# Kernel tuning notes

Hardware: AMD Instinct MI355X
Metric: run time of the kernel (lower is better)

Reference implementation:

```python
import jax, jax.numpy as jnp
import numpy as np
from jax import lax

B, N, C = 16, 16384, 90      # batch, anchors, classes
K = 100                      # per-class pre-NMS top-k
MAX_DET = 100                # final detections per image
IOU_THR = 0.5
SCORE_THR = 0.05


def setup_inputs() -> dict:
    key = jax.random.key(0)
    k1, k2, k3, k4 = jax.random.split(key, 4)
    box_encodings = jax.random.normal(k1, (B, N, 4), dtype=jnp.float32) * 0.5
    class_logits = jax.random.normal(k2, (B, N, C), dtype=jnp.float32) * 2.0 - 3.0
    # anchors as [ymin,xmin,ymax,xmax] in normalized coords
    centers = jax.random.uniform(k3, (N, 2), dtype=jnp.float32)             # (cy,cx)
    sizes = jax.random.uniform(k4, (N, 2), dtype=jnp.float32, minval=0.05, maxval=0.3)
    anchors = jnp.concatenate([centers - sizes / 2, centers + sizes / 2], axis=-1)
    return {"box_encodings": box_encodings, "class_logits": class_logits, "anchors": anchors}


def decode_boxes(enc, anchors):
    ymin, xmin, ymax, xmax = [anchors[:, i] for i in range(4)]
    ha, wa = ymax - ymin, xmax - xmin
    cya, cxa = (ymin + ymax) / 2, (xmin + xmax) / 2
    ty, tx, th, tw = enc[..., 0] / 10.0, enc[..., 1] / 10.0, enc[..., 2] / 5.0, enc[..., 3] / 5.0
    cy = ty * ha + cya
    cx = tx * wa + cxa
    h = jnp.exp(th) * ha
    w = jnp.exp(tw) * wa
    boxes = jnp.stack([cy - h / 2, cx - w / 2, cy + h / 2, cx + w / 2], axis=-1)
    return jnp.clip(boxes, 0.0, 1.0)  # [..., N, 4]


def pairwise_iou(b):  # b: [K,4]
    area = jnp.maximum(b[:, 2] - b[:, 0], 0) * jnp.maximum(b[:, 3] - b[:, 1], 0)
    iy = jnp.maximum(jnp.minimum(b[:, None, 2], b[None, :, 2]) - jnp.maximum(b[:, None, 0], b[None, :, 0]), 0)
    ix = jnp.maximum(jnp.minimum(b[:, None, 3], b[None, :, 3]) - jnp.maximum(b[:, None, 1], b[None, :, 1]), 0)
    inter = iy * ix
    union = area[:, None] + area[None, :] - inter
    return inter / jnp.maximum(union, 1e-8)


def nms_one_class(boxes, scores_c):  # boxes [N,4], scores_c [N]
    vals, idx = lax.top_k(scores_c, K)           # sorted descending
    bk = boxes[idx]                               # [K,4]
    iou = pairwise_iou(bk)                        # [K,K]
    def step(keep, i):
        supp = jnp.any(keep & (iou[i] >= IOU_THR))
        ki = (vals[i] > SCORE_THR) & (~supp)
        return keep.at[i].set(ki), None
    keep, _ = lax.scan(step, jnp.zeros((K,), bool), jnp.arange(K))
    return bk, vals * keep                        # suppressed -> score 0


def postprocess_one(boxes, scores):  # boxes [N,4], scores [N,C]
    bx_ck, sc_ck = jax.vmap(nms_one_class, in_axes=(None, 1))(boxes, scores)  # [C,K,4],[C,K]
    cls_ck = jnp.broadcast_to(jnp.arange(C, dtype=jnp.float32)[:, None], (C, K))
    sc_f = sc_ck.reshape(-1)
    fsc, fidx = lax.top_k(sc_f, MAX_DET)
    fbx = bx_ck.reshape(-1, 4)[fidx]
    fcl = cls_ck.reshape(-1)[fidx]
    return jnp.concatenate([fbx, fcl[:, None], fsc[:, None]], axis=-1)  # [MAX_DET, 6]


def reference(box_encodings, class_logits, anchors):
    boxes = decode_boxes(box_encodings, anchors)       # [B,N,4]
    scores = jax.nn.sigmoid(class_logits)              # [B,N,C]
    combined = jax.vmap(postprocess_one)(boxes, scores)  # [B,MAX_DET,6] = boxes|class|score
    return combined
```

## Files before the change

kernel.cpp:

```cpp
#include <hip/hip_runtime.h>
#include <stdint.h>
#include <math.h>

#define B_ 16
#define NN 16384
#define C_ 90
#define KSEL 100
#define MAXD 100
#define MFLAT (C_ * KSEL)
#define NPAIR 128
#define ZKEY 0x80000000u


__device__ __forceinline__ uint32_t fkey(float f) {
  uint32_t u = __float_as_uint(f);
  return (u & 0x80000000u) ? ~u : (u | 0x80000000u);
}
__device__ __forceinline__ float keyinv(uint32_t k) {
  uint32_t u = (k & 0x80000000u) ? (k & 0x7FFFFFFFu) : ~k;
  return __uint_as_float(u);
}

__device__ __forceinline__ uint32_t blockSum512(uint32_t v, uint32_t* red, uint32_t* s_total) {
  int tid = threadIdx.x;
#pragma unroll
  for (int o = 32; o > 0; o >>= 1) v += __shfl_down(v, o, 64);
  if ((tid & 63) == 0) red[tid >> 6] = v;
  __syncthreads();
  if (tid == 0) {
    uint32_t s = 0;
#pragma unroll
    for (int i = 0; i < 8; ++i) s += red[i];
    *s_total = s;
  }
  __syncthreads();
  return *s_total;
}

__device__ __forceinline__ uint32_t blockSum256(uint32_t v, uint32_t* red, uint32_t* s_total) {
  int tid = threadIdx.x;
#pragma unroll
  for (int o = 32; o > 0; o >>= 1) v += __shfl_down(v, o, 64);
  if ((tid & 63) == 0) red[tid >> 6] = v;
  __syncthreads();
  if (tid == 0) *s_total = red[0] + red[1] + red[2] + red[3];
  __syncthreads();
  return *s_total;
}

__global__ __launch_bounds__(256) void transpose_key16_kernel(const float* __restrict__ logits,
                                                              uint16_t* __restrict__ keys16T) {
  __shared__ uint32_t tile[128 * 91];
  int b = blockIdx.y;
  int n0 = blockIdx.x * 128;
  const float4* src4 = reinterpret_cast<const float4*>(logits + ((size_t)b * NN + n0) * C_);
  for (int p = threadIdx.x; p < 2880; p += 256) {
    float4 v = src4[p];
    int e = p * 4;
    float vv[4] = {v.x, v.y, v.z, v.w};
#pragma unroll
    for (int j = 0; j < 4; ++j) {
      int ee = e + j;
      tile[(ee / C_) * 91 + (ee % C_)] = fkey(vv[j]);
    }
  }
  __syncthreads();
  uint16_t* dstb = keys16T + (size_t)b * C_ * NN + n0;
  for (int q = threadIdx.x; q < C_ * 16; q += 256) {
    int c = q >> 4, g = q & 15;
    int nn2 = g * 8;
    uint4 o;
    o.x = (tile[(nn2 + 0) * 91 + c] >> 16) | (tile[(nn2 + 1) * 91 + c] & 0xFFFF0000u);
    o.y = (tile[(nn2 + 2) * 91 + c] >> 16) | (tile[(nn2 + 3) * 91 + c] & 0xFFFF0000u);
    o.z = (tile[(nn2 + 4) * 91 + c] >> 16) | (tile[(nn2 + 5) * 91 + c] & 0xFFFF0000u);
    o.w = (tile[(nn2 + 6) * 91 + c] >> 16) | (tile[(nn2 + 7) * 91 + c] & 0xFFFF0000u);
    reinterpret_cast<uint4*>(dstb + (size_t)c * NN)[g] = o;
  }
}

template <int TR>
__global__ __launch_bounds__(512, 4) void select_kernel(
    const uint16_t* __restrict__ keys16T,
    const float* __restrict__ logits,
    uint32_t* __restrict__ candPacked,
    uint32_t* __restrict__ candCount) {
  __shared__ uint32_t hist[2048];
  __shared__ uint32_t sc[512];
  __shared__ uint32_t ws8[64];
  __shared__ int s_bsel;
  __shared__ uint32_t s_Sincl, s_Sexcl;
  __shared__ uint32_t red[8];
  __shared__ uint32_t s_total;
  __shared__ uint32_t s_cnt;

  const int c = blockIdx.x, b = blockIdx.y;
  const int tid = threadIdx.x;

  uint32_t keyw[16];
  if (TR) {
    const uint4* src4 = reinterpret_cast<const uint4*>(keys16T + ((size_t)b * C_ + c) * NN);
#pragma unroll
    for (int q = 0; q < 4; ++q) {
      uint4 kv = src4[q * 512 + tid];
      keyw[4 * q + 0] = kv.x; keyw[4 * q + 1] = kv.y;
      keyw[4 * q + 2] = kv.z; keyw[4 * q + 3] = kv.w;
    }
  } else {
    const float* src = logits + (size_t)b * NN * C_ + c;
#pragma unroll
    for (int m = 0; m < 16; ++m) {
      uint32_t i0 = (uint32_t)((((m >> 2) * 512 + tid) * 8) + ((m & 3) * 2));
      uint32_t klo = fkey(src[(size_t)i0 * C_]) >> 16;
      uint32_t khi = fkey(src[(size_t)(i0 + 1) * C_]) >> 16;
      keyw[m] = klo | (khi << 16);
    }
  }

  reinterpret_cast<uint4*>(hist)[tid] = make_uint4(0u, 0u, 0u, 0u);
  __syncthreads();
#pragma unroll
  for (int m = 0; m < 16; ++m) {
    uint32_t w = keyw[m];
    atomicAdd(&hist[(w & 0xFFFFu) >> 5], 1u);
    atomicAdd(&hist[w >> 21], 1u);
  }
  __syncthreads();

  uint32_t m_above = 0;
  uint32_t need = 100u;
  uint32_t cut16 = 0;
  int found = 0;
  int tiepath = 0;
  uint32_t V16 = 0, Texact = NN - 1;

  {
    uint32_t h0 = hist[4 * tid], h1 = hist[4 * tid + 1];
    uint32_t h2 = hist[4 * tid + 2], h3 = hist[4 * tid + 3];
    sc[tid] = h0 + h1 + h2 + h3;
    if (tid == 0) s_bsel = -1;
    __syncthreads();
    if (tid < 64) {
      uint32_t w = 0;
      int base = tid * 8;
#pragma unroll
      for (int i = 0; i < 8; ++i) w += sc[base + i];
#pragma unroll
      for (int off = 1; off < 64; off <<= 1) {
        uint32_t v = __shfl_down(w, off, 64);
        if (tid + off < 64) w += v;
      }
      ws8[tid] = w;
    }
    __syncthreads();
    {
      int g = tid >> 3;
      uint32_t above = (g < 63) ? ws8[g + 1] : 0u;
      for (int j = (g << 3) + 7; j > tid; --j) above += sc[j];
      uint32_t run = above;
      int best = -1;
      uint32_t bi = 0, be = 0;
      uint32_t hh[4] = {h0, h1, h2, h3};
#pragma unroll
      for (int p = 3; p >= 0; --p) {
        uint32_t h = hh[p];
        run += h;
        if (best < 0 && run >= need) { best = 4 * tid + p; bi = run; be = run - h; }
      }
      if (best >= 0) atomicMax(&s_bsel, best);
      __syncthreads();
      if (best >= 0 && best == s_bsel) { s_Sincl = bi; s_Sexcl = be; }
    }
    __syncthreads();

    uint32_t bsel = (uint32_t)s_bsel;
    uint32_t Sincl = s_Sincl, Sexcl = s_Sexcl;
    if (Sincl <= (uint32_t)NPAIR) {
      cut16 = bsel << 5;
      found = 1;
    } else {
      m_above = Sexcl;
      need = 100u - m_above;
      __syncthreads();
      if (tid < 8) reinterpret_cast<uint4*>(hist)[tid] = make_uint4(0u, 0u, 0u, 0u);
      __syncthreads();
#pragma unroll
      for (int m = 0; m < 16; ++m) {
        uint32_t w = keyw[m];
        uint32_t klo = w & 0xFFFFu, khi = w >> 16;
        if ((klo >> 5) == bsel) atomicAdd(&hist[klo & 31u], 1u);
        if ((khi >> 5) == bsel) atomicAdd(&hist[khi & 31u], 1u);
      }
      __syncthreads();
      uint32_t run = 0;
      int b1 = -1;
      uint32_t Si = 0, Se = 0;
      for (int p = 31; p >= 0; --p) {
        uint32_t h = hist[p];
        run += h;
        if (b1 < 0 && run >= need) { b1 = p; Si = run; Se = run - h; }
      }
      uint32_t cutv = (bsel << 5) | (uint32_t)b1;
      if (m_above + Si <= (uint32_t)NPAIR) {
        cut16 = cutv;
        found = 1;
      } else {
        tiepath = 1;
        V16 = cutv;
        m_above += Se;
        uint32_t r = 100u - m_above;
        uint32_t lo2 = 0, hi2 = NN - 1;
        while (lo2 < hi2) {
          uint32_t mid2 = lo2 + ((hi2 - lo2) >> 1);
          uint32_t cnt = 0;
#pragma unroll
          for (int m = 0; m < 16; ++m) {
            uint32_t w = keyw[m];
            uint32_t i0 = (uint32_t)((((m >> 2) * 512 + tid) * 8) + ((m & 3) * 2));
            cnt += ((w & 0xFFFFu) == V16 && i0 <= mid2) ? 1u : 0u;
            cnt += ((w >> 16) == V16 && (i0 + 1) <= mid2) ? 1u : 0u;
          }
          uint32_t tot = blockSum512(cnt, red, &s_total);
          if (tot >= r) hi2 = mid2; else lo2 = mid2 + 1;
        }
        Texact = lo2;
      }
    }
  }

  if (tid == 0) s_cnt = 0;
  __syncthreads();
  uint32_t* outp = candPacked + (size_t)(b * C_ + c) * NPAIR;
#pragma unroll
  for (int m = 0; m < 16; ++m) {
    uint32_t w = keyw[m];
    uint32_t i0 = (uint32_t)((((m >> 2) * 512 + tid) * 8) + ((m & 3) * 2));
    uint32_t klo = w & 0xFFFFu, khi = w >> 16;
    bool t0 = tiepath ? (klo > V16 || (klo == V16 && i0 <= Texact)) : (klo >= cut16);
    bool t1 = tiepath ? (khi > V16 || (khi == V16 && (i0 + 1) <= Texact)) : (khi >= cut16);
    if (t0) {
      uint32_t p = atomicAdd(&s_cnt, 1u);
      if (p < (uint32_t)NPAIR) outp[p] = (klo << 16) | i0;
    }
    if (t1) {
      uint32_t p = atomicAdd(&s_cnt, 1u);
      if (p < (uint32_t)NPAIR) outp[p] = (khi << 16) | (i0 + 1);
    }
  }
  __syncthreads();
  if (tid == 0) candCount[b * C_ + c] = (s_cnt > (uint32_t)NPAIR) ? (uint32_t)NPAIR : s_cnt;
}

__global__ __launch_bounds__(128, 4) void sort_nms_kernel(
    const uint32_t* __restrict__ candPacked,
    const uint32_t* __restrict__ candCount,
    const float* __restrict__ logits,
    const float* __restrict__ enc,
    const float* __restrict__ anchors,
    float* __restrict__ candBox,
    float* __restrict__ candScore) {
  __shared__ unsigned long long ck[NPAIR];
  __shared__ float s_vals[KSEL];
  __shared__ float s_boxv[KSEL][5];
  __shared__ float s_area[KSEL];
  __shared__ uint32_t smask[KSEL][4];
  __shared__ unsigned long long s_keepw[2];

  const int c = blockIdx.x, b = blockIdx.y;
  const int tid = threadIdx.x;
  const int bc = b * C_ + c;

  uint32_t cnt = candCount[bc];
  unsigned long long ckv = 0ull;
  if (tid < (int)cnt) {
    uint32_t v = candPacked[(size_t)bc * NPAIR + tid];
    int n = (int)(v & 0x3FFFu);
    float x = logits[((size_t)b * NN + n) * C_ + c];
    float s = 1.0f / (1.0f + expf(-x));
    ckv = ((unsigned long long)fkey(s) << 32) | (unsigned long long)(~(uint32_t)n);
  }
  ck[tid] = ckv;
  __syncthreads();

  for (int kk = 2; kk <= 128; kk <<= 1) {
    for (int j = kk >> 1; j > 0; j >>= 1) {
      int ixj = tid ^ j;
      if (ixj > tid) {
        unsigned long long a = ck[tid], bb2 = ck[ixj];
        if ((a < bb2) == ((tid & kk) == 0)) { ck[tid] = bb2; ck[ixj] = a; }
      }
      __syncthreads();
    }
  }

  if (tid < KSEL) {
    unsigned long long keyv = ck[tid];
    uint32_t hk = (uint32_t)(keyv >> 32);
    int n = (int)(~(uint32_t)(keyv & 0xFFFFFFFFull)) & (NN - 1);
    s_vals[tid] = keyinv(hk);
    float4 e = reinterpret_cast<const float4*>(enc)[(size_t)b * NN + n];
    float4 a = reinterpret_cast<const float4*>(anchors)[n];
    float ha = a.z - a.x, wa = a.w - a.y;
    float cya = (a.x + a.z) * 0.5f, cxa = (a.y + a.w) * 0.5f;
    float cy = (e.x / 10.0f) * ha + cya;
    float cx = (e.y / 10.0f) * wa + cxa;
    float h = expf(e.z / 5.0f) * ha;
    float w = expf(e.w / 5.0f) * wa;
    float y1 = fminf(fmaxf(cy - h * 0.5f, 0.0f), 1.0f);
    float x1 = fminf(fmaxf(cx - w * 0.5f, 0.0f), 1.0f);
    float y2 = fminf(fmaxf(cy + h * 0.5f, 0.0f), 1.0f);
    float x2 = fminf(fmaxf(cx + w * 0.5f, 0.0f), 1.0f);
    s_boxv[tid][0] = y1; s_boxv[tid][1] = x1; s_boxv[tid][2] = y2; s_boxv[tid][3] = x2;
    s_area[tid] = fmaxf(y2 - y1, 0.0f) * fmaxf(x2 - x1, 0.0f);
    smask[tid][0] = 0; smask[tid][1] = 0; smask[tid][2] = 0; smask[tid][3] = 0;
  }
  __syncthreads();

  for (int p = tid; p < (KSEL * (KSEL - 1)) / 2; p += 128) {
    int j = (int)((1.0f + sqrtf(1.0f + 8.0f * (float)p)) * 0.5f);
    while (j * (j - 1) / 2 > p) --j;
    while ((j + 1) * j / 2 <= p) ++j;
    int i = p - j * (j - 1) / 2;
    float iy1 = s_boxv[i][0], ix1 = s_boxv[i][1], iy2 = s_boxv[i][2], ix2 = s_boxv[i][3];
    float jy1 = s_boxv[j][0], jx1 = s_boxv[j][1], jy2 = s_boxv[j][2], jx2 = s_boxv[j][3];
    float ta = fmaxf(fminf(iy2, jy2) - fmaxf(iy1, jy1), 0.0f) *
               fmaxf(fminf(ix2, jx2) - fmaxf(ix1, jx1), 0.0f);
    float un = fmaxf(s_area[i] + s_area[j] - ta, 1e-8f);
    if (ta / un >= 0.5f) atomicOr(&smask[i][j >> 5], 1u << (j & 31));
  }
  __syncthreads();

  if (tid < 64) {
    int L = tid;
    unsigned long long r0 = (unsigned long long)smask[L][0] |
                            ((unsigned long long)smask[L][1] << 32);
    unsigned long long r1 = (unsigned long long)smask[L][2] |
                            ((unsigned long long)smask[L][3] << 32);
    unsigned long long r2 = 0, r3 = 0;
    if (L < KSEL - 64) {
      r2 = (unsigned long long)smask[L + 64][0] | ((unsigned long long)smask[L + 64][1] << 32);
      r3 = (unsigned long long)smask[L + 64][2] | ((unsigned long long)smask[L + 64][3] << 32);
    }
    unsigned long long vm0 = __ballot(s_vals[L] > 0.05f);
    unsigned long long vm1 = __ballot((L + 64 < KSEL) ? (s_vals[L + 64] > 0.05f) : false);
    unsigned long long supp0 = 0, supp1 = 0, k0 = 0, k1 = 0;
    for (int j = 0; j < KSEL; ++j) {
      unsigned long long rl, rh;
      bool pass;
      if (j < 64) {
        rl = __shfl(r0, j); rh = __shfl(r1, j);
        pass = ((vm0 >> j) & 1ull) && !((supp0 >> j) & 1ull);
      } else {
        rl = __shfl(r2, j - 64); rh = __shfl(r3, j - 64);
        pass = ((vm1 >> (j - 64)) & 1ull) && !((supp1 >> (j - 64)) & 1ull);
      }
      if (pass) {
        supp0 |= rl; supp1 |= rh;
        if (j < 64) k0 |= 1ull << j; else k1 |= 1ull << (j - 64);
      }
    }
    if (tid == 0) { s_keepw[0] = k0; s_keepw[1] = k1; }
  }
  __syncthreads();

  if (tid < KSEL) {
    bool kept = (tid < 64) ? ((s_keepw[0] >> tid) & 1ull)
                           : ((s_keepw[1] >> (tid - 64)) & 1ull);
    size_t base = (size_t)bc * KSEL + tid;
    candScore[base] = kept ? s_vals[tid] : 0.0f;
    float* cb = candBox + base * 4;
    cb[0] = s_boxv[tid][0]; cb[1] = s_boxv[tid][1];
    cb[2] = s_boxv[tid][2]; cb[3] = s_boxv[tid][3];
  }
}

#define FSLOT 36
__global__ __launch_bounds__(256) void final_topk_kernel(
    const float* __restrict__ candScore,
    const float* __restrict__ candBox,
    float* __restrict__ out) {
  __shared__ uint32_t hist[2048 * 8];
  __shared__ uint32_t sc[256];
  __shared__ uint32_t ws4[64];
  __shared__ int s_bsel;
  __shared__ uint32_t s_Sincl, s_Sexcl;
  __shared__ uint32_t red[4];
  __shared__ uint32_t s_total;
  __shared__ uint32_t s_cnt;
  __shared__ unsigned long long ck[128];

  int b = blockIdx.x, tid = threadIdx.x;
  const float* src = candScore + (size_t)b * MFLAT;

  uint32_t key[FSLOT];
#pragma unroll
  for (int q = 0; q < FSLOT; ++q) {
    int idx = q * 256 + tid;
    key[q] = (idx < MFLAT) ? fkey(src[idx]) : 0u;
  }

  uint32_t nzc = 0;
#pragma unroll
  for (int q = 0; q < FSLOT; ++q) nzc += (key[q] > ZKEY) ? 1u : 0u;
  uint32_t nz = blockSum256(nzc, red, &s_total);

  uint32_t cutHi = 0, m_above = 0, cut32 = 0;
  int found = 0, tiepath = 0;
  uint32_t V32 = 0, Texact = (uint32_t)(MFLAT - 1);
  uint32_t tie_r = 0;

  if (nz < 100u) {
    tiepath = 1;
    V32 = ZKEY;
    tie_r = 100u - nz;
  } else {
    const int stripe = tid & 7;
    for (int lvl = 0; lvl < 3; ++lvl) {
      const int shiftLo = (lvl == 0) ? 21 : (lvl == 1) ? 10 : 0;
      const uint32_t mask = (lvl == 2) ? 0x3FFu : 0x7FFu;
      const int nbits = (lvl == 2) ? 10 : 11;

      for (int i = tid; i < 4096; i += 256)
        reinterpret_cast<uint4*>(hist)[i] = make_uint4(0u, 0u, 0u, 0u);
      __syncthreads();
#pragma unroll
      for (int q = 0; q < FSLOT; ++q) {
        uint32_t k = key[q];
        bool in = (k > ZKEY) && ((lvl == 0) ? true : ((k >> (shiftLo + nbits)) == cutHi));
        if (in) atomicAdd(&hist[(((k >> shiftLo) & mask) << 3) + stripe], 1u);
      }
      __syncthreads();

      const uint32_t need = 100u - m_above;

      uint32_t h[8];
#pragma unroll
      for (int i = 0; i < 8; ++i) {
        uint4 a = reinterpret_cast<uint4*>(hist)[(8 * tid + i) * 2];
        uint4 d = reinterpret_cast<uint4*>(hist)[(8 * tid + i) * 2 + 1];
        h[i] = a.x + a.y + a.z + a.w + d.x + d.y + d.z + d.w;
      }
      sc[tid] = h[0] + h[1] + h[2] + h[3] + h[4] + h[5] + h[6] + h[7];
      if (tid == 0) s_bsel = -1;
      __syncthreads();
      if (tid < 64) {
        uint32_t w = sc[4 * tid] + sc[4 * tid + 1] + sc[4 * tid + 2] + sc[4 * tid + 3];
#pragma unroll
        for (int off = 1; off < 64; off <<= 1) {
          uint32_t v = __shfl_down(w, off, 64);
          if (tid + off < 64) w += v;
        }
        ws4[tid] = w;
      }
      __syncthreads();
      {
        int g = tid >> 2;
        uint32_t above = (g < 63) ? ws4[g + 1] : 0u;
        for (int j = (g << 2) + 3; j > tid; --j) above += sc[j];
        uint32_t run = above;
        int best = -1;
        uint32_t bi = 0, be = 0;
#pragma unroll
        for (int p = 7; p >= 0; --p) {
          run += h[p];
          if (best < 0 && run >= need) { best = 8 * tid + p; bi = run; be = run - h[p]; }
        }
        if (best >= 0) atomicMax(&s_bsel, best);
        __syncthreads();
        if (best >= 0 && best == s_bsel) { s_Sincl = bi; s_Sexcl = be; }
      }
      __syncthreads();

      uint32_t bsel = (uint32_t)s_bsel;
      cutHi = (cutHi << nbits) | bsel;
      if (m_above + s_Sincl <= 128u) {
        cut32 = cutHi << shiftLo;
        found = 1;
        break;
      }
      m_above += s_Sexcl;
      __syncthreads();
    }

    if (!found) {
      tiepath = 1;
      V32 = cutHi;
      tie_r = 100u - m_above;
    }
  }

  if (tiepath) {
    uint32_t lo2 = 0, hi2 = (uint32_t)(MFLAT - 1);
    while (lo2 < hi2) {
      uint32_t mid2 = lo2 + ((hi2 - lo2) >> 1);
      uint32_t cnt = 0;
#pragma unroll
      for (int q = 0; q < FSLOT; ++q) {
        uint32_t idx = (uint32_t)(q * 256 + tid);
        cnt += (key[q] == V32 && idx <= mid2) ? 1u : 0u;
      }
      uint32_t tot = blockSum256(cnt, red, &s_total);
      if (tot >= tie_r) hi2 = mid2; else lo2 = mid2 + 1;
    }
    Texact = lo2;
  }

  if (tid == 0) s_cnt = 0;
  __syncthreads();
#pragma unroll
  for (int q = 0; q < FSLOT; ++q) {
    uint32_t k = key[q];
    uint32_t idx = (uint32_t)(q * 256 + tid);
    bool take = tiepath ? (k > V32 || (k == V32 && idx <= Texact))
                        : (k > ZKEY && k >= cut32);
    if (take) {
      uint32_t p = atomicAdd(&s_cnt, 1u);
      if (p < 128u)
        ck[p] = ((unsigned long long)k << 32) | (unsigned long long)(~idx);
    }
  }
  __syncthreads();
  if (tid < 128 && (uint32_t)tid >= s_cnt) ck[tid] = 0ull;
  __syncthreads();

  for (int kk = 2; kk <= 128; kk <<= 1) {
    for (int j = kk >> 1; j > 0; j >>= 1) {
      if (tid < 128) {
        int ixj = tid ^ j;
        if (ixj > tid) {
          unsigned long long a = ck[tid], bb = ck[ixj];
          if ((a < bb) == ((tid & kk) == 0)) { ck[tid] = bb; ck[ixj] = a; }
        }
      }
      __syncthreads();
    }
  }

  if (tid < MAXD) {
    unsigned long long keyv = ck[tid];
    int f = (int)(~(uint32_t)(keyv & 0xFFFFFFFFull));
    int c = f / KSEL;
    float sc2 = keyinv((uint32_t)(keyv >> 32));
    const float* cb = candBox + ((size_t)b * MFLAT + f) * 4;
    float* o = out + ((size_t)b * MAXD + tid) * 6;
    o[0] = cb[0]; o[1] = cb[1]; o[2] = cb[2]; o[3] = cb[3];
    o[4] = (float)c; o[5] = sc2;
  }
}

extern "C" void kernel_launch(void* const* d_in, const int* in_sizes, int n_in,
                              void* d_out, int out_size, void* d_ws, size_t ws_size,
                              hipStream_t stream) {
  const float* enc = (const float*)d_in[0];
  const float* logits = (const float*)d_in[1];
  const float* anchors = (const float*)d_in[2];
  float* out = (float*)d_out;
  char* ws = (char*)d_ws;

  size_t off = 0;
  float* candBox = (float*)(ws + off);   off += (size_t)B_ * C_ * KSEL * 4 * sizeof(float);
  float* candScore = (float*)(ws + off); off += (size_t)B_ * C_ * KSEL * sizeof(float);
  uint32_t* candPacked = (uint32_t*)(ws + off);
  off += (size_t)B_ * C_ * NPAIR * sizeof(uint32_t);
  uint32_t* candCount = (uint32_t*)(ws + off); off += (size_t)B_ * C_ * sizeof(uint32_t);
  off = (off + 255) & ~(size_t)255;
  uint16_t* keys16T = (uint16_t*)(ws + off);
  size_t needT = off + (size_t)B_ * C_ * NN * sizeof(uint16_t);
  int transposed = (ws_size >= needT) ? 1 : 0;

  if (transposed) {
    transpose_key16_kernel<<<dim3(NN / 128, B_), 256, 0, stream>>>(logits, keys16T);
    select_kernel<1><<<dim3(C_, B_), 512, 0, stream>>>(keys16T, logits, candPacked, candCount);
  } else {
    select_kernel<0><<<dim3(C_, B_), 512, 0, stream>>>(keys16T, logits, candPacked, candCount);
  }

  sort_nms_kernel<<<dim3(C_, B_), 128, 0, stream>>>(candPacked, candCount, logits,
                                                    enc, anchors, candBox, candScore);

  final_topk_kernel<<<B_, 256, 0, stream>>>(candScore, candBox, out);
}
```

Baseline: 135.3 us.

## Widen final top-k to 512 threads with shared-memory keys and per-wave histograms

The final per-image top-k kernel now runs 512 threads instead of 256. It stages the 9000 candidate keys in shared memory instead of a 36-entry register array, and replaces the 8-way striped histogram with one 2048-bin histogram per wavefront that is summed during the scan. The aim is more parallelism and lower register pressure in a kernel that only launches 16 blocks, and less atomic contention per bin. In exchange it adds about 70KB of shared-memory traffic and a reduction across the eight wave histograms.

```diff
diff --git a/kernel.cpp b/kernel.cpp
--- a/kernel.cpp
+++ b/kernel.cpp
@@ -33,17 +33,6 @@
     for (int i = 0; i < 8; ++i) s += red[i];
     *s_total = s;
   }
-  __syncthreads();
-  return *s_total;
-}
-
-__device__ __forceinline__ uint32_t blockSum256(uint32_t v, uint32_t* red, uint32_t* s_total) {
-  int tid = threadIdx.x;
-#pragma unroll
-  for (int o = 32; o > 0; o >>= 1) v += __shfl_down(v, o, 64);
-  if ((tid & 63) == 0) red[tid >> 6] = v;
-  __syncthreads();
-  if (tid == 0) *s_total = red[0] + red[1] + red[2] + red[3];
   __syncthreads();
   return *s_total;
 }
@@ -373,35 +362,37 @@
   }
 }
 
-#define FSLOT 36
-__global__ __launch_bounds__(256) void final_topk_kernel(
+#define FT_NT 512
+#define FT_SLOTS 18
+#define FT_NW 8
+__global__ __launch_bounds__(FT_NT) void final_topk_kernel(
     const float* __restrict__ candScore,
     const float* __restrict__ candBox,
     float* __restrict__ out) {
-  __shared__ uint32_t hist[2048 * 8];
-  __shared__ uint32_t sc[256];
-  __shared__ uint32_t ws4[64];
+  __shared__ uint32_t skey[FT_NT * FT_SLOTS];
+  __shared__ uint32_t hist[FT_NW * 2048];
+  __shared__ uint32_t sc[512];
+  __shared__ uint32_t ws8[64];
   __shared__ int s_bsel;
   __shared__ uint32_t s_Sincl, s_Sexcl;
-  __shared__ uint32_t red[4];
+  __shared__ uint32_t red[8];
   __shared__ uint32_t s_total;
   __shared__ uint32_t s_cnt;
   __shared__ unsigned long long ck[128];
 
   int b = blockIdx.x, tid = threadIdx.x;
+  const int wid = tid >> 6;
   const float* src = candScore + (size_t)b * MFLAT;
 
-  uint32_t key[FSLOT];
-#pragma unroll
-  for (int q = 0; q < FSLOT; ++q) {
-    int idx = q * 256 + tid;
-    key[q] = (idx < MFLAT) ? fkey(src[idx]) : 0u;
-  }
-
   uint32_t nzc = 0;
-#pragma unroll
-  for (int q = 0; q < FSLOT; ++q) nzc += (key[q] > ZKEY) ? 1u : 0u;
-  uint32_t nz = blockSum256(nzc, red, &s_total);
+  for (int q = 0; q < FT_SLOTS; ++q) {
+    int idx = q * FT_NT + tid;
+    uint32_t k = (idx < MFLAT) ? fkey(src[idx]) : 0u;
+    skey[idx] = k;
+    nzc += (k > ZKEY) ? 1u : 0u;
+  }
+  __syncthreads();
+  uint32_t nz = blockSum512(nzc, red, &s_total);
 
   uint32_t cutHi = 0, m_above = 0, cut32 = 0;
   int found = 0, tiepath = 0;
@@ -413,56 +404,59 @@
     V32 = ZKEY;
     tie_r = 100u - nz;
   } else {
-    const int stripe = tid & 7;
     for (int lvl = 0; lvl < 3; ++lvl) {
       const int shiftLo = (lvl == 0) ? 21 : (lvl == 1) ? 10 : 0;
       const uint32_t mask = (lvl == 2) ? 0x3FFu : 0x7FFu;
       const int nbits = (lvl == 2) ? 10 : 11;
 
-      for (int i = tid; i < 4096; i += 256)
+      for (int i = tid; i < FT_NW * 512; i += FT_NT)
         reinterpret_cast<uint4*>(hist)[i] = make_uint4(0u, 0u, 0u, 0u);
       __syncthreads();
-#pragma unroll
-      for (int q = 0; q < FSLOT; ++q) {
-        uint32_t k = key[q];
+      uint32_t* myh = hist + wid * 2048;
+      for (int q = 0; q < FT_SLOTS; ++q) {
+        uint32_t k = skey[q * FT_NT + tid];
         bool in = (k > ZKEY) && ((lvl == 0) ? true : ((k >> (shiftLo + nbits)) == cutHi));
-        if (in) atomicAdd(&hist[(((k >> shiftLo) & mask) << 3) + stripe], 1u);
+        if (in) atomicAdd(&myh[(k >> shiftLo) & mask], 1u);
       }
       __syncthreads();
 
       const uint32_t need = 100u - m_above;
 
-      uint32_t h[8];
-#pragma unroll
-      for (int i = 0; i < 8; ++i) {
-        uint4 a = reinterpret_cast<uint4*>(hist)[(8 * tid + i) * 2];
-        uint4 d = reinterpret_cast<uint4*>(hist)[(8 * tid + i) * 2 + 1];
-        h[i] = a.x + a.y + a.z + a.w + d.x + d.y + d.z + d.w;
-      }
-      sc[tid] = h[0] + h[1] + h[2] + h[3] + h[4] + h[5] + h[6] + h[7];
+      uint32_t h0 = 0, h1 = 0, h2 = 0, h3 = 0;
+#pragma unroll
+      for (int w = 0; w < FT_NW; ++w) {
+        uint4 a = *reinterpret_cast<const uint4*>(hist + w * 2048 + 4 * tid);
+        h0 += a.x; h1 += a.y; h2 += a.z; h3 += a.w;
+      }
+      sc[tid] = h0 + h1 + h2 + h3;
       if (tid == 0) s_bsel = -1;
       __syncthreads();
       if (tid < 64) {
-        uint32_t w = sc[4 * tid] + sc[4 * tid + 1] + sc[4 * tid + 2] + sc[4 * tid + 3];
+        uint32_t w = 0;
+        int base = tid * 8;
+#pragma unroll
+        for (int i = 0; i < 8; ++i) w += sc[base + i];
 #pragma unroll
         for (int off = 1; off < 64; off <<= 1) {
           uint32_t v = __shfl_down(w, off, 64);
           if (tid + off < 64) w += v;
         }
-        ws4[tid] = w;
+        ws8[tid] = w;
       }
       __syncthreads();
       {
-        int g = tid >> 2;
-        uint32_t above = (g < 63) ? ws4[g + 1] : 0u;
-        for (int j = (g << 2) + 3; j > tid; --j) above += sc[j];
+        int g = tid >> 3;
+        uint32_t above = (g < 63) ? ws8[g + 1] : 0u;
+        for (int j = (g << 3) + 7; j > tid; --j) above += sc[j];
         uint32_t run = above;
         int best = -1;
         uint32_t bi = 0, be = 0;
-#pragma unroll
-        for (int p = 7; p >= 0; --p) {
-          run += h[p];
-          if (best < 0 && run >= need) { best = 8 * tid + p; bi = run; be = run - h[p]; }
+        uint32_t hh[4] = {h0, h1, h2, h3};
+#pragma unroll
+        for (int p = 3; p >= 0; --p) {
+          uint32_t h = hh[p];
+          run += h;
+          if (best < 0 && run >= need) { best = 4 * tid + p; bi = run; be = run - h; }
         }
         if (best >= 0) atomicMax(&s_bsel, best);
         __syncthreads();
@@ -493,12 +487,11 @@
     while (lo2 < hi2) {
       uint32_t mid2 = lo2 + ((hi2 - lo2) >> 1);
       uint32_t cnt = 0;
-#pragma unroll
-      for (int q = 0; q < FSLOT; ++q) {
-        uint32_t idx = (uint32_t)(q * 256 + tid);
-        cnt += (key[q] == V32 && idx <= mid2) ? 1u : 0u;
-      }
-      uint32_t tot = blockSum256(cnt, red, &s_total);
+      for (int q = 0; q < FT_SLOTS; ++q) {
+        uint32_t idx = (uint32_t)(q * FT_NT + tid);
+        cnt += (skey[idx] == V32 && idx <= mid2) ? 1u : 0u;
+      }
+      uint32_t tot = blockSum512(cnt, red, &s_total);
       if (tot >= tie_r) hi2 = mid2; else lo2 = mid2 + 1;
     }
     Texact = lo2;
@@ -506,10 +499,9 @@
 
   if (tid == 0) s_cnt = 0;
   __syncthreads();
-#pragma unroll
-  for (int q = 0; q < FSLOT; ++q) {
-    uint32_t k = key[q];
-    uint32_t idx = (uint32_t)(q * 256 + tid);
+  for (int q = 0; q < FT_SLOTS; ++q) {
+    uint32_t idx = (uint32_t)(q * FT_NT + tid);
+    uint32_t k = skey[idx];
     bool take = tiepath ? (k > V32 || (k == V32 && idx <= Texact))
                         : (k > ZKEY && k >= cut32);
     if (take) {
@@ -577,5 +569,5 @@
   sort_nms_kernel<<<dim3(C_, B_), 128, 0, stream>>>(candPacked, candCount, logits,
                                                     enc, anchors, candBox, candScore);
 
-  final_topk_kernel<<<B_, 256, 0, stream>>>(candScore, candBox, out);
-}
+  final_topk_kernel<<<B_, FT_NT, 0, stream>>>(candScore, candBox, out);
+}
```

Result: no change. 134.4 us (-0.7%).
